# Optimization experiments

Measured on AMD Instinct MI355X. Metric: run time of the kernel, lower is better.

The kernel has to match this reference:

```python
import jax, jax.numpy as jnp
import numpy as np
import math

B, H, L = 8, 256, 4096
C = 1            # channels
D_STATE = 64
DD = D_STATE // 2  # d = 32
DT_MIN, DT_MAX = 1e-3, 1e-1


def setup_inputs() -> dict:
    key = jax.random.key(0)
    ks = jax.random.split(key, 6)
    u = jax.random.normal(ks[0], (B, H, L), dtype=jnp.float32)
    # analytic init matching the torch module
    h_scale = jnp.exp(jnp.arange(H, dtype=jnp.float32) / H * math.log(DT_MAX / DT_MIN))  # (H,)
    angles = jnp.arange(DD, dtype=jnp.float32) * jnp.float32(np.pi)                      # (DD,)
    theta = jnp.einsum('c,h,d->chd', jnp.ones((C,), jnp.float32), h_scale, angles)       # (C,H,DD)
    a = -jnp.broadcast_to(h_scale[None, :, None], (C, H, DD)).astype(jnp.float32)        # (C,H,DD)
    D = jax.random.normal(ks[1], (C, H), dtype=jnp.float32)
    b_p = jax.random.normal(ks[2], (C, H, DD), dtype=jnp.float32)
    c_p = jax.random.normal(ks[3], (C, H, DD), dtype=jnp.float32)
    x0 = jax.random.normal(ks[4], (C, H, DD), dtype=jnp.float32)
    return {"u": u, "theta": theta, "a": a, "D": D, "b_p": b_p, "c_p": c_p, "x0": x0}


def fft_conv(u, f):
    # u: (B,H,L), f: (C,H,L) -> (B,C,H,L) causal conv via zero-padded FFT
    l = u.shape[-1]
    n = 2 * l
    u_f = jnp.fft.rfft(u, n=n)          # (B,H,n//2+1)
    f_f = jnp.fft.rfft(f, n=n)          # (C,H,n//2+1)
    y_f = jnp.einsum('bhl,chl->bchl', u_f, f_f)
    return jnp.fft.irfft(y_f, n=n)[..., :l]


def reference(u, theta, a, D, b_p, c_p, x0):
    l = u.shape[-1]
    T = 1.0 / (l - 1)
    zk = T * jnp.arange(l, dtype=jnp.float32)            # (L,)
    zk4 = zk[None, None, :, None]                         # (1,1,L,1)
    ls = -jnp.abs(a) + 1j * theta                         # (C,H,DD) complex
    term_0 = (jnp.exp(ls * T) - 1.0) / ls                 # (C,H,DD)
    # base_term: (C,H,L,DD)
    base_term = (2.0 * term_0[:, :, None, :] * jnp.exp(ls[:, :, None, :] * zk4)).real
    q = b_p * c_p                                         # (C,H,DD)
    f = jnp.einsum('chd,chld->chl', q, base_term)         # (C,H,L)
    y = fft_conv(u, f)                                    # (B,C,H,L)
    y = y + jnp.einsum('bhl,ch->bchl', u, D)
    # initial-condition term
    cos_term = 2.0 * T * jnp.exp(-jnp.abs(a)[:, :, None, :] * zk4) * jnp.cos(theta[:, :, None, :] * zk4)
    init = jnp.einsum('chd,chld->chl', 2.0 * (c_p * x0), cos_term)  # (C,H,L)
    y = y + init[None]                                    # broadcast over batch
    b = y.shape[0]
    return y.reshape(b, -1, l)                            # (B, C*H, L)
```

## Files before the change

### kernel.cpp

```cpp
#include <hip/hip_runtime.h>

#define BB 8
#define HH 256
#define LL 4096
#define STR 72

typedef __attribute__((ext_vector_type(8))) short short8;
typedef __attribute__((ext_vector_type(4))) float f32x4;

static __device__ inline unsigned short f2bf(float x) {
    union { float f; unsigned u; } v; v.f = x;
    unsigned r = v.u + 0x7fffu + ((v.u >> 16) & 1u);
    return (unsigned short)(r >> 16);
}
static __device__ inline float bf2f(unsigned short us) {
    union { unsigned u; float f; } v; v.u = ((unsigned)us) << 16; return v.f;
}

#define CMUL(or_, oi_, ar_, ai_, br_, bi_) do { \
    float _tr = fmaf((ar_), (br_), -(ai_) * (bi_)); \
    float _ti = fmaf((ar_), (bi_), (ai_) * (br_)); \
    (or_) = _tr; (oi_) = _ti; } while (0)

__global__ __launch_bounds__(256, 4) void s4_fused_kernel(
    const float* __restrict__ u, const float* __restrict__ theta,
    const float* __restrict__ a, const float* __restrict__ Dp,
    const float* __restrict__ b_p, const float* __restrict__ c_p,
    const float* __restrict__ x0, float* __restrict__ out)
{
    const int tid = threadIdx.x;
    const int blk = blockIdx.x;
    const int hh  = blk >> 2;
    const int bp  = blk & 3;

    __shared__ __align__(16) short UsA[64 * STR];
    __shared__ __align__(16) short UsB[64 * STR];
    __shared__ __align__(16) short EQ[64 * STR];
    __shared__ __align__(16) float Seg[32 * 18];
    __shared__ unsigned short h_sb[64];

    const int d    = tid & 31;
    const int g    = tid >> 5;
    const int ln   = tid & 63;
    const int m0   = (tid >> 6) << 4;
    const int rowi = ln & 15;
    const int quad = ln >> 4;

    const float* up0 = u + ((((size_t)(bp * 2) * HH) + hh) << 12);
    const float* up1 = u + ((((size_t)(bp * 2 + 1) * HH) + hh) << 12);
    float4 v0[4];
    #pragma unroll
    for (int jj = 0; jj < 4; ++jj)
        v0[jj] = ((const float4*)up0)[tid + (jj << 8)];

    const float T = 1.0f / (LL - 1);
    const float lr = a[hh * 32 + d];
    const float li = theta[hh * 32 + d];
    float sn, cS;
    sincosf(li * T, &sn, &cS);
    const float er = expf(lr * T);
    const float Rr = er * cS, Ri = er * sn;
    const float den = lr * lr + li * li;
    const float t0r = ((Rr - 1.f) * lr + Ri * li) / den;
    const float t0i = (Ri * lr - (Rr - 1.f) * li) / den;
    const float qq  = b_p[hh * 32 + d] * c_p[hh * 32 + d];
    const float wre = 2.f * qq * t0r, wim = 2.f * qq * t0i;
    const float vv  = 4.f * T * c_p[hh * 32 + d] * x0[hh * 32 + d];
    const float Dh  = Dp[hh];

    float r2r, r2i, r4r, r4i, r8r, r8i, r16r, r16i, r32r, r32i;
    CMUL(r2r, r2i, Rr, Ri, Rr, Ri);
    CMUL(r4r, r4i, r2r, r2i, r2r, r2i);
    CMUL(r8r, r8i, r4r, r4i, r4r, r4i);
    CMUL(r16r, r16i, r8r, r8i, r8r, r8i);
    CMUL(r32r, r32i, r16r, r16i, r16r, r16i);

    {
        float pr = 1.f, pi = 0.f;
        if (g & 1) CMUL(pr, pi, pr, pi, r8r, r8i);
        if (g & 2) CMUL(pr, pi, pr, pi, r16r, r16i);
        if (g & 4) CMUL(pr, pi, pr, pi, r32r, r32i);
        #pragma unroll
        for (int k8 = 0; k8 < 8; ++k8) {
            const int k = (g << 3) + k8;
            EQ[k * STR + d]            = (short)f2bf(pr);
            EQ[k * STR + 32 + d]       = (short)f2bf(-pi);
            UsB[d * STR + (63 - k)]        = (short)f2bf(pr);
            UsB[(32 + d) * STR + (63 - k)] = (short)f2bf(pi);
            float hk = fmaf(wre, pr, -wim * pi);
            hk += __shfl_xor(hk, 1);
            hk += __shfl_xor(hk, 2);
            hk += __shfl_xor(hk, 4);
            hk += __shfl_xor(hk, 8);
            hk += __shfl_xor(hk, 16);
            if (d == 0) h_sb[k] = f2bf(hk);
            CMUL(pr, pi, pr, pi, Rr, Ri);
        }
    }

    float Ar, Ai, wrr, wri;
    CMUL(Ar, Ai, r32r, r32i, r32r, r32i);
    CMUL(wrr, wri, wre, wim, Rr, Ri);
    float S8r, S8i, S16r, S16i, S32r, S32i;
    {
        float b1r, b1i, b2r, b2i;
        CMUL(b1r, b1i, Ar, Ai, Ar, Ai);
        CMUL(b2r, b2i, b1r, b1i, b1r, b1i);
        CMUL(S8r, S8i, b2r, b2i, b2r, b2i);
        CMUL(S16r, S16i, S8r, S8i, S8r, S8i);
        CMUL(S32r, S32i, S16r, S16i, S16r, S16i);
    }

    #pragma unroll
    for (int jj = 0; jj < 4; ++jj) {
        const int v  = tid + (jj << 8);
        const int c  = v >> 4;
        const int t0 = (v & 15) << 2;
        uint2 pk;
        pk.x = (unsigned)f2bf(v0[jj].x) | ((unsigned)f2bf(v0[jj].y) << 16);
        pk.y = (unsigned)f2bf(v0[jj].z) | ((unsigned)f2bf(v0[jj].w) << 16);
        *(uint2*)&UsA[c * STR + t0] = pk;
    }
    float4 v1[4];
    #pragma unroll
    for (int jj = 0; jj < 4; ++jj)
        v1[jj] = ((const float4*)up1)[tid + (jj << 8)];
    __syncthreads();

    short8 aH[2], aP[2], aR[2];
    #pragma unroll
    for (int kh = 0; kh < 2; ++kh) {
        const int off = (m0 + rowi) * STR + (kh << 5) + (quad << 3);
        aP[kh] = *(const short8*)&UsB[off];
        aR[kh] = *(const short8*)&EQ[off];
    }
    #pragma unroll
    for (int kh = 0; kh < 2; ++kh) {
        short8 hv;
        #pragma unroll
        for (int j = 0; j < 8; ++j) {
            const int dt = (m0 + rowi) - ((kh << 5) + (quad << 3) + j);
            hv[j] = (dt >= 0) ? (short)h_sb[dt] : (short)0;
        }
        aH[kh] = hv;
    }
    __syncthreads();

    #pragma unroll
    for (int it = 0; it < 2; ++it) {
        short* Us = it ? UsB : UsA;

        f32x4 accY[4], accE[4];
        #pragma unroll
        for (int nt = 0; nt < 4; ++nt) {
            accY[nt] = (f32x4){0.f, 0.f, 0.f, 0.f};
            accE[nt] = (f32x4){0.f, 0.f, 0.f, 0.f};
        }
        #pragma unroll
        for (int kh = 0; kh < 2; ++kh) {
            const int k0 = kh << 5;
            #pragma unroll
            for (int nt = 0; nt < 4; ++nt) {
                const short8 bU = *(const short8*)&Us[((nt << 4) + rowi) * STR + k0 + (quad << 3)];
                accY[nt] = __builtin_amdgcn_mfma_f32_16x16x32_bf16(aH[kh], bU, accY[nt], 0, 0, 0);
                accE[nt] = __builtin_amdgcn_mfma_f32_16x16x32_bf16(aP[kh], bU, accE[nt], 0, 0, 0);
            }
        }

        #pragma unroll
        for (int nt = 0; nt < 4; ++nt) {
            uint2 pk;
            pk.x = (unsigned)f2bf(accE[nt][0]) | ((unsigned)f2bf(accE[nt][1]) << 16);
            pk.y = (unsigned)f2bf(accE[nt][2]) | ((unsigned)f2bf(accE[nt][3]) << 16);
            *(uint2*)&EQ[((nt << 4) + rowi) * STR + m0 + (quad << 2)] = pk;
        }

        if (it == 0) {
            #pragma unroll
            for (int jj = 0; jj < 4; ++jj) {
                const int v  = tid + (jj << 8);
                const int c  = v >> 4;
                const int t0 = (v & 15) << 2;
                uint2 pk;
                pk.x = (unsigned)f2bf(v1[jj].x) | ((unsigned)f2bf(v1[jj].y) << 16);
                pk.y = (unsigned)f2bf(v1[jj].z) | ((unsigned)f2bf(v1[jj].w) << 16);
                *(uint2*)&UsB[c * STR + t0] = pk;
            }
        }
        __syncthreads();

        const int cb = g << 3;
        float Er[8], Ei[8];
        {
            float Sr = 0.f, Si = 0.f;
            #pragma unroll
            for (int i = 0; i < 8; ++i) {
                const int c = cb + i;
                Er[i] = bf2f((unsigned short)EQ[c * STR + d]);
                Ei[i] = bf2f((unsigned short)EQ[c * STR + 32 + d]);
                const float nr = fmaf(Ar, Sr, fmaf(-Ai, Si, Er[i]));
                const float ni = fmaf(Ar, Si, fmaf(Ai, Sr, Ei[i]));
                Sr = nr; Si = ni;
            }
            Seg[d * 18 + (g << 1)]     = Sr;
            Seg[d * 18 + (g << 1) + 1] = Si;
        }
        __syncthreads();

        {
            float offr = 0.f, offi = 0.f;
            #pragma unroll
            for (int gp = 0; gp < 7; ++gp) {
                const float2 sg = *(const float2*)&Seg[d * 18 + (gp << 1)];
                const float nr = fmaf(S8r, offr, fmaf(-S8i, offi, sg.x));
                const float ni = fmaf(S8r, offi, fmaf(S8i, offr, sg.y));
                const bool take = gp < g;
                offr = take ? nr : offr;
                offi = take ? ni : offi;
            }
            float Gr = vv, Gi = 0.f;
            if (g & 1) { float nr, ni; CMUL(nr, ni, Gr, Gi, S8r, S8i);   Gr = nr; Gi = ni; }
            if (g & 2) { float nr, ni; CMUL(nr, ni, Gr, Gi, S16r, S16i); Gr = nr; Gi = ni; }
            if (g & 4) { float nr, ni; CMUL(nr, ni, Gr, Gi, S32r, S32i); Gr = nr; Gi = ni; }
            float Sr = offr, Si = offi;
            #pragma unroll
            for (int i = 0; i < 8; ++i) {
                const int c = cb + i;
                const float Qr = fmaf(wrr, Sr, fmaf(-wri, Si, Gr));
                const float Qi = fmaf(wrr, Si, fmaf(wri, Sr, Gi));
                EQ[c * STR + d]      = (short)f2bf(Qr);
                EQ[c * STR + 32 + d] = (short)f2bf(Qi);
                const float nr = fmaf(Ar, Sr, fmaf(-Ai, Si, Er[i]));
                const float ni = fmaf(Ar, Si, fmaf(Ai, Sr, Ei[i]));
                Sr = nr; Si = ni;
                float nGr, nGi;
                CMUL(nGr, nGi, Ar, Ai, Gr, Gi);
                Gr = nGr; Gi = nGi;
            }
        }
        __syncthreads();

        #pragma unroll
        for (int kh = 0; kh < 2; ++kh) {
            const int k0 = kh << 5;
            #pragma unroll
            for (int nt = 0; nt < 4; ++nt) {
                const short8 bQ = *(const short8*)&EQ[((nt << 4) + rowi) * STR + k0 + (quad << 3)];
                accY[nt] = __builtin_amdgcn_mfma_f32_16x16x32_bf16(aR[kh], bQ, accY[nt], 0, 0, 0);
            }
        }

        float* op = out + ((((size_t)(bp * 2 + it) * HH) + hh) << 12);
        #pragma unroll
        for (int nt = 0; nt < 4; ++nt) {
            const int c    = (nt << 4) + rowi;
            const int toff = m0 + (quad << 2);
            const uint2 uu = *(const uint2*)&Us[c * STR + toff];
            float4 res;
            res.x = fmaf(Dh, bf2f((unsigned short)(uu.x & 0xffffu)), accY[nt][0]);
            res.y = fmaf(Dh, bf2f((unsigned short)(uu.x >> 16)),     accY[nt][1]);
            res.z = fmaf(Dh, bf2f((unsigned short)(uu.y & 0xffffu)), accY[nt][2]);
            res.w = fmaf(Dh, bf2f((unsigned short)(uu.y >> 16)),     accY[nt][3]);
            *(float4*)&op[c * 64 + toff] = res;
        }
        if (it == 0) __syncthreads();
    }
}

extern "C" void kernel_launch(void* const* d_in, const int* in_sizes, int n_in,
                              void* d_out, int out_size, void* d_ws, size_t ws_size,
                              hipStream_t stream) {
    const float* u     = (const float*)d_in[0];
    const float* theta = (const float*)d_in[1];
    const float* a     = (const float*)d_in[2];
    const float* Dp    = (const float*)d_in[3];
    const float* b_p   = (const float*)d_in[4];
    const float* c_p   = (const float*)d_in[5];
    const float* x0    = (const float*)d_in[6];
    float* out = (float*)d_out;
    (void)d_ws; (void)ws_size;

    hipLaunchKernelGGL(s4_fused_kernel, dim3(HH * 4), dim3(256), 0, stream,
                       u, theta, a, Dp, b_p, c_p, x0, out);
}
```

Before: 101.3 us.

## Compute power-matrix fragments in registers and add separate Em buffer to drop barriers

The aP MFMA operand fragments were built by storing the R power table into LDS (UsB) and reading it back. They are now computed directly in registers, using shuffles of per-lane power values and repeated complex multiplies. A new LDS buffer Em holds the chunk-end states instead of overwriting EQ, which lets two __syncthreads be removed: the one after the fragment loads and the one at the end of the first iteration. The intent is fewer barriers and less LDS traffic. The cost is extra ALU work, more LDS footprint (possibly lower occupancy), and slightly different bf16 rounding of the powers.

```diff
diff --git a/kernel.cpp b/kernel.cpp
--- a/kernel.cpp
+++ b/kernel.cpp
@@ -36,6 +36,7 @@
     __shared__ __align__(16) short UsA[64 * STR];
     __shared__ __align__(16) short UsB[64 * STR];
     __shared__ __align__(16) short EQ[64 * STR];
+    __shared__ __align__(16) short Em[64 * STR];
     __shared__ __align__(16) float Seg[32 * 18];
     __shared__ unsigned short h_sb[64];
 
@@ -85,8 +86,6 @@
             const int k = (g << 3) + k8;
             EQ[k * STR + d]            = (short)f2bf(pr);
             EQ[k * STR + 32 + d]       = (short)f2bf(-pi);
-            UsB[d * STR + (63 - k)]        = (short)f2bf(pr);
-            UsB[(32 + d) * STR + (63 - k)] = (short)f2bf(pi);
             float hk = fmaf(wre, pr, -wim * pi);
             hk += __shfl_xor(hk, 1);
             hk += __shfl_xor(hk, 2);
@@ -131,7 +130,6 @@
     #pragma unroll
     for (int kh = 0; kh < 2; ++kh) {
         const int off = (m0 + rowi) * STR + (kh << 5) + (quad << 3);
-        aP[kh] = *(const short8*)&UsB[off];
         aR[kh] = *(const short8*)&EQ[off];
     }
     #pragma unroll
@@ -144,7 +142,39 @@
         }
         aH[kh] = hv;
     }
-    __syncthreads();
+    {
+        const int  row  = m0 + rowi;
+        const int  dp   = row & 31;
+        const bool isIm = row >= 32;
+        const float R1r = __shfl(Rr,   dp), R1i = __shfl(Ri,   dp);
+        const float P8r = __shfl(r8r,  dp), P8i = __shfl(r8i,  dp);
+        const float P16r = __shfl(r16r, dp), P16i = __shfl(r16i, dp);
+        const float P32r = __shfl(r32r, dp), P32i = __shfl(r32i, dp);
+        #pragma unroll
+        for (int kh = 0; kh < 2; ++kh) {
+            const int col0 = (kh << 5) + (quad << 3);
+            const int e7   = 63 - col0 - 7;
+            const int eb   = e7 >> 3;
+            float pr = 1.f, pi = 0.f;
+            {
+                float tr, ti;
+                CMUL(tr, ti, pr, pi, P8r, P8i);
+                pr = (eb & 1) ? tr : pr;  pi = (eb & 1) ? ti : pi;
+                CMUL(tr, ti, pr, pi, P16r, P16i);
+                pr = (eb & 2) ? tr : pr;  pi = (eb & 2) ? ti : pi;
+                CMUL(tr, ti, pr, pi, P32r, P32i);
+                pr = (eb & 4) ? tr : pr;  pi = (eb & 4) ? ti : pi;
+            }
+            short8 pv;
+            pv[7] = (short)f2bf(isIm ? pi : pr);
+            #pragma unroll
+            for (int j = 6; j >= 0; --j) {
+                CMUL(pr, pi, pr, pi, R1r, R1i);
+                pv[j] = (short)f2bf(isIm ? pi : pr);
+            }
+            aP[kh] = pv;
+        }
+    }
 
     #pragma unroll
     for (int it = 0; it < 2; ++it) {
@@ -172,7 +202,7 @@
             uint2 pk;
             pk.x = (unsigned)f2bf(accE[nt][0]) | ((unsigned)f2bf(accE[nt][1]) << 16);
             pk.y = (unsigned)f2bf(accE[nt][2]) | ((unsigned)f2bf(accE[nt][3]) << 16);
-            *(uint2*)&EQ[((nt << 4) + rowi) * STR + m0 + (quad << 2)] = pk;
+            *(uint2*)&Em[((nt << 4) + rowi) * STR + m0 + (quad << 2)] = pk;
         }
 
         if (it == 0) {
@@ -196,8 +226,8 @@
             #pragma unroll
             for (int i = 0; i < 8; ++i) {
                 const int c = cb + i;
-                Er[i] = bf2f((unsigned short)EQ[c * STR + d]);
-                Ei[i] = bf2f((unsigned short)EQ[c * STR + 32 + d]);
+                Er[i] = bf2f((unsigned short)Em[c * STR + d]);
+                Ei[i] = bf2f((unsigned short)Em[c * STR + 32 + d]);
                 const float nr = fmaf(Ar, Sr, fmaf(-Ai, Si, Er[i]));
                 const float ni = fmaf(Ar, Si, fmaf(Ai, Sr, Ei[i]));
                 Sr = nr; Si = ni;
@@ -263,7 +293,6 @@
             res.w = fmaf(Dh, bf2f((unsigned short)(uu.y >> 16)),     accY[nt][3]);
             *(float4*)&op[c * 64 + toff] = res;
         }
-        if (it == 0) __syncthreads();
     }
 }
 
```

Measured after the change: 101.3 us. No clear change (-0.0%).
